# Performance work log

Measured on AMD Instinct MI355X. Metric: run time of the kernel, lower is better.

## Reference

```python
import jax, jax.numpy as jnp
import numpy as np

N = 100_000   # total nodes in batched graph
E = 800_000   # total edges
D = 64        # in_dim
H = 64        # hidden_dim
C = 10        # out_dim (num classes)
L = 3         # num_layers
G = 500       # graphs in batch
EPS = 1e-5    # BatchNorm eps


def setup_inputs() -> dict:
    key = jax.random.key(0)
    ks = jax.random.split(key, 12)
    feat = jax.random.normal(ks[0], (N, D), dtype=jnp.float32)
    src = jax.random.randint(ks[1], (E,), 0, N, dtype=jnp.int32)
    dst = jax.random.randint(ks[2], (E,), 0, N, dtype=jnp.int32)
    node2graph = jnp.sort(jax.random.randint(ks[3], (N,), 0, G, dtype=jnp.int32))
    # stacked GCN layer params (in_dim == hidden_dim so all layers share shape)
    Ws = jax.random.normal(ks[4], (L, H, H), dtype=jnp.float32) * 0.1
    bs = jax.random.normal(ks[5], (L, H), dtype=jnp.float32) * 0.01
    gammas = 1.0 + 0.1 * jax.random.normal(ks[6], (L, H), dtype=jnp.float32)
    betas = 0.1 * jax.random.normal(ks[7], (L, H), dtype=jnp.float32)
    means = 0.1 * jax.random.normal(ks[8], (L, H), dtype=jnp.float32)
    vars_ = jax.random.uniform(ks[9], (L, H), dtype=jnp.float32) + 0.5
    Wc = jax.random.normal(ks[10], (H, C), dtype=jnp.float32) * 0.1
    bc = jax.random.normal(ks[11], (C,), dtype=jnp.float32) * 0.01
    return {"feat": feat, "src": src, "dst": dst, "node2graph": node2graph,
            "Ws": Ws, "bs": bs, "gammas": gammas, "betas": betas,
            "means": means, "vars_": vars_, "Wc": Wc, "bc": bc}


def reference(feat, src, dst, node2graph, Ws, bs, gammas, betas, means, vars_, Wc, bc):
    h = feat
    for l in range(L):
        # dgl copy_src + sum: aggregate source features at destination nodes
        m = jax.ops.segment_sum(h[src], dst, num_segments=N)  # [N, H]
        h = m @ Ws[l] + bs[l]                                  # Linear
        # BatchNorm1d (eval mode, running stats)
        h = (h - means[l]) * (gammas[l] / jnp.sqrt(vars_[l] + EPS)) + betas[l]
        h = jax.nn.elu(h)
    logits = h @ Wc + bc                    # classify(h)
    logp = jax.nn.log_softmax(logits, axis=1)
    Hent = -jnp.sum(jnp.exp(logp) * logp, axis=1)   # entropy per node
    lam = 1.0 - Hent / jnp.max(Hent)                # lambda_list
    # ragged per-graph weighted sum pooling
    pooled = jax.ops.segment_sum(lam[:, None] * h, node2graph, num_segments=G)  # [G, H]
    return pooled @ Wc + bc                 # final classify (dropout eval = id)
```

## Files before the change

kernel.cpp:

```cpp
#include <hip/hip_runtime.h>
#include <hip/hip_bf16.h>
#include <math.h>

#define NNODES 100000
#define NEDGES 800000
#define HDIM 64
#define CDIM 10
#define NGRAPH 500
#define CAP 24
#define OVFCAP 16384
#define BN_EPS 1e-5f
#define TN 64

typedef __attribute__((ext_vector_type(8))) short short8;
typedef __attribute__((ext_vector_type(4))) float f32x4;

__device__ __forceinline__ float bflo(unsigned u){ return __uint_as_float(u << 16); }
__device__ __forceinline__ float bfhi(unsigned u){ return __uint_as_float(u & 0xFFFF0000u); }
__device__ __forceinline__ unsigned f2bf(float f){
    unsigned u = __float_as_uint(f);
    u += 0x7FFFu + ((u >> 16) & 1u);
    return u >> 16;
}

__global__ void cvt_feat(const float4* __restrict__ F, uint4* __restrict__ B) {
    int i = blockIdx.x * 256 + threadIdx.x;
    float4 a = F[2*i], b = F[2*i+1];
    uint4 o;
    o.x = f2bf(a.x) | (f2bf(a.y) << 16);
    o.y = f2bf(a.z) | (f2bf(a.w) << 16);
    o.z = f2bf(b.x) | (f2bf(b.y) << 16);
    o.w = f2bf(b.z) | (f2bf(b.w) << 16);
    B[i] = o;
}

__global__ void fill_buckets(const int* __restrict__ src, const int* __restrict__ dst,
                             unsigned* __restrict__ cnt, int* __restrict__ csr,
                             unsigned* __restrict__ ovfcnt, int* __restrict__ ovf) {
    int e = blockIdx.x * blockDim.x + threadIdx.x;
    if (e >= NEDGES) return;
    int d = dst[e];
    unsigned slot = atomicAdd(&cnt[d], 1u);
    if (slot < CAP) {
        csr[(size_t)d * CAP + slot] = src[e];
    } else {
        unsigned o = atomicAdd(ovfcnt, 1u);
        if (o < OVFCAP) { ovf[2*o] = src[e]; ovf[2*o+1] = d; }
    }
}

__global__ __launch_bounds__(256, 6) void layer_fused(
        const unsigned* __restrict__ hb, const unsigned* __restrict__ cnt,
        const int* __restrict__ csr, const unsigned* __restrict__ ovfcnt,
        const int* __restrict__ ovf,
        const float* __restrict__ Ws, const float* __restrict__ bs,
        const float* __restrict__ gammas, const float* __restrict__ betas,
        const float* __restrict__ means, const float* __restrict__ vars_,
        int layer, unsigned short* __restrict__ out16) {
    __shared__ unsigned short Mb[TN][72];
    __shared__ unsigned short Wt[HDIM][72];
    __shared__ float Scl[HDIM], Shl[HDIM];
    int tid = threadIdx.x;
    int base = blockIdx.x * TN;

    const float* Wg = Ws + (size_t)layer*HDIM*HDIM;
    #pragma unroll
    for (int r = 0; r < 16; ++r) {
        int f = tid + 256*r;
        int k = f >> 6, c = f & 63;
        Wt[c][k] = (unsigned short)f2bf(Wg[f]);
    }
    if (tid < HDIM) {
        int c = tid;
        float b  = bs[layer*HDIM + c];
        float gm = gammas[layer*HDIM + c];
        float be = betas[layer*HDIM + c];
        float mu = means[layer*HDIM + c];
        float vv = vars_[layer*HDIM + c];
        float s  = gm * rsqrtf(vv + BN_EPS);
        Scl[c] = s;
        Shl[c] = (b - mu) * s + be;
    }

    int grp = tid >> 3;
    int sub = tid & 7;
    const uint4* h4 = (const uint4*)hb;
    unsigned novf = *ovfcnt; if (novf > OVFCAP) novf = OVFCAP;
    #pragma unroll
    for (int i = 0; i < 2; ++i) {
        int row = grp + 32*i;
        int node = base + row;
        float a0=0,a1=0,a2=0,a3=0,a4=0,a5=0,a6=0,a7=0;
        if (node < NNODES) {
            unsigned deg = cnt[node]; if (deg > CAP) deg = CAP;
            const int* ed = csr + (size_t)node * CAP;
            unsigned e = 0;
            for (; e + 4 <= deg; e += 4) {
                int s0 = ed[e], s1 = ed[e+1], s2 = ed[e+2], s3 = ed[e+3];
                uint4 v0 = h4[(size_t)s0*8 + sub];
                uint4 v1 = h4[(size_t)s1*8 + sub];
                uint4 v2 = h4[(size_t)s2*8 + sub];
                uint4 v3 = h4[(size_t)s3*8 + sub];
                a0 += bflo(v0.x)+bflo(v1.x)+bflo(v2.x)+bflo(v3.x);
                a1 += bfhi(v0.x)+bfhi(v1.x)+bfhi(v2.x)+bfhi(v3.x);
                a2 += bflo(v0.y)+bflo(v1.y)+bflo(v2.y)+bflo(v3.y);
                a3 += bfhi(v0.y)+bfhi(v1.y)+bfhi(v2.y)+bfhi(v3.y);
                a4 += bflo(v0.z)+bflo(v1.z)+bflo(v2.z)+bflo(v3.z);
                a5 += bfhi(v0.z)+bfhi(v1.z)+bfhi(v2.z)+bfhi(v3.z);
                a6 += bflo(v0.w)+bflo(v1.w)+bflo(v2.w)+bflo(v3.w);
                a7 += bfhi(v0.w)+bfhi(v1.w)+bfhi(v2.w)+bfhi(v3.w);
            }
            for (; e < deg; ++e) {
                uint4 v = h4[(size_t)ed[e]*8 + sub];
                a0 += bflo(v.x); a1 += bfhi(v.x);
                a2 += bflo(v.y); a3 += bfhi(v.y);
                a4 += bflo(v.z); a5 += bfhi(v.z);
                a6 += bflo(v.w); a7 += bfhi(v.w);
            }
            if (novf) {
                for (unsigned o = 0; o < novf; ++o) {
                    if (ovf[2*o+1] == node) {
                        uint4 v = h4[(size_t)ovf[2*o]*8 + sub];
                        a0 += bflo(v.x); a1 += bfhi(v.x);
                        a2 += bflo(v.y); a3 += bfhi(v.y);
                        a4 += bflo(v.z); a5 += bfhi(v.z);
                        a6 += bflo(v.w); a7 += bfhi(v.w);
                    }
                }
            }
        }
        uint4 p;
        p.x = f2bf(a0) | (f2bf(a1) << 16);
        p.y = f2bf(a2) | (f2bf(a3) << 16);
        p.z = f2bf(a4) | (f2bf(a5) << 16);
        p.w = f2bf(a6) | (f2bf(a7) << 16);
        *(uint4*)&Mb[row][sub*8] = p;
    }
    __syncthreads();

    int w  = tid >> 6;
    int l  = tid & 63;
    int lr = l & 15;
    int lq = l >> 4;
    short8 a0 = *(const short8*)&Mb[w*16 + lr][lq*8];
    short8 a1 = *(const short8*)&Mb[w*16 + lr][32 + lq*8];
    f32x4 acc0 = {0.f,0.f,0.f,0.f}, acc1 = acc0, acc2 = acc0, acc3 = acc0;
    {
        short8 b0 = *(const short8*)&Wt[ 0 + lr][lq*8];
        short8 b1 = *(const short8*)&Wt[ 0 + lr][32 + lq*8];
        acc0 = __builtin_amdgcn_mfma_f32_16x16x32_bf16(a0, b0, acc0, 0, 0, 0);
        acc0 = __builtin_amdgcn_mfma_f32_16x16x32_bf16(a1, b1, acc0, 0, 0, 0);
    }
    {
        short8 b0 = *(const short8*)&Wt[16 + lr][lq*8];
        short8 b1 = *(const short8*)&Wt[16 + lr][32 + lq*8];
        acc1 = __builtin_amdgcn_mfma_f32_16x16x32_bf16(a0, b0, acc1, 0, 0, 0);
        acc1 = __builtin_amdgcn_mfma_f32_16x16x32_bf16(a1, b1, acc1, 0, 0, 0);
    }
    {
        short8 b0 = *(const short8*)&Wt[32 + lr][lq*8];
        short8 b1 = *(const short8*)&Wt[32 + lr][32 + lq*8];
        acc2 = __builtin_amdgcn_mfma_f32_16x16x32_bf16(a0, b0, acc2, 0, 0, 0);
        acc2 = __builtin_amdgcn_mfma_f32_16x16x32_bf16(a1, b1, acc2, 0, 0, 0);
    }
    {
        short8 b0 = *(const short8*)&Wt[48 + lr][lq*8];
        short8 b1 = *(const short8*)&Wt[48 + lr][32 + lq*8];
        acc3 = __builtin_amdgcn_mfma_f32_16x16x32_bf16(a0, b0, acc3, 0, 0, 0);
        acc3 = __builtin_amdgcn_mfma_f32_16x16x32_bf16(a1, b1, acc3, 0, 0, 0);
    }

    #pragma unroll
    for (int t = 0; t < 4; ++t) {
        f32x4 a = (t==0)?acc0:(t==1)?acc1:(t==2)?acc2:acc3;
        int col = t*16 + lr;
        float s = Scl[col], sh = Shl[col];
        #pragma unroll
        for (int r = 0; r < 4; ++r) {
            int node = base + w*16 + lq*4 + r;
            if (node < NNODES) {
                float y = a[r]*s + sh;
                y = (y > 0.f) ? y : expm1f(y);
                out16[(size_t)node*HDIM + col] = (unsigned short)f2bf(y);
            }
        }
    }
}

__global__ __launch_bounds__(256) void classify_bf16(
        const uint4* __restrict__ h4, const float* __restrict__ Wc,
        const float* __restrict__ bc, float* __restrict__ Hent,
        unsigned* __restrict__ maxH) {
    __shared__ float Wl[HDIM*11];
    __shared__ float bl[CDIM];
    __shared__ float wmax[4];
    int tid = threadIdx.x;
    for (int idx = tid; idx < HDIM*CDIM; idx += 256)
        Wl[(idx/CDIM)*11 + (idx%CDIM)] = Wc[idx];
    if (tid < CDIM) bl[tid] = bc[tid];
    __syncthreads();

    int node = blockIdx.x * 32 + (tid >> 3);
    int sub  = tid & 7;
    uint4 v = h4[(size_t)node*8 + sub];
    float h[8];
    h[0]=bflo(v.x); h[1]=bfhi(v.x); h[2]=bflo(v.y); h[3]=bfhi(v.y);
    h[4]=bflo(v.z); h[5]=bfhi(v.z); h[6]=bflo(v.w); h[7]=bfhi(v.w);

    float lg[CDIM];
    #pragma unroll
    for (int c = 0; c < CDIM; ++c) lg[c] = 0.f;
    #pragma unroll
    for (int k = 0; k < 8; ++k) {
        const float* wr = &Wl[(sub*8 + k)*11];
        float x = h[k];
        #pragma unroll
        for (int c = 0; c < CDIM; ++c) lg[c] += x * wr[c];
    }
    #pragma unroll
    for (int m = 1; m < 8; m <<= 1)
        #pragma unroll
        for (int c = 0; c < CDIM; ++c) lg[c] += __shfl_xor(lg[c], m, 64);
    #pragma unroll
    for (int c = 0; c < CDIM; ++c) lg[c] += bl[c];

    float mx = lg[0];
    #pragma unroll
    for (int c = 1; c < CDIM; ++c) mx = fmaxf(mx, lg[c]);
    float se = 0.f, dot = 0.f;
    #pragma unroll
    for (int c = 0; c < CDIM; ++c) { float e = expf(lg[c]-mx); se += e; dot += e*lg[c]; }
    float Hv = (mx + logf(se)) - dot/se;
    Hv = fmaxf(Hv, 0.f);
    if (sub == 0) Hent[node] = Hv;

    float m8 = Hv;
    #pragma unroll
    for (int m = 8; m < 64; m <<= 1) m8 = fmaxf(m8, __shfl_xor(m8, m, 64));
    if ((tid & 63) == 0) wmax[tid >> 6] = m8;
    __syncthreads();
    if (tid == 0) {
        float mm = fmaxf(fmaxf(wmax[0], wmax[1]), fmaxf(wmax[2], wmax[3]));
        atomicMax(maxH, __float_as_uint(mm));
    }
}

__global__ void pool_final_bf16(const unsigned* __restrict__ H2, const float* __restrict__ Hent,
                                const unsigned* __restrict__ maxH, const int* __restrict__ n2g,
                                const float* __restrict__ Wc, const float* __restrict__ bc,
                                float* __restrict__ out) {
    __shared__ float partial[8][HDIM];
    __shared__ float pooled[HDIM];
    int g = blockIdx.x;
    int tid = threadIdx.x;

    int lo = 0, hi = NNODES;
    while (lo < hi) { int mid = (lo+hi) >> 1; if (n2g[mid] < g) lo = mid+1; else hi = mid; }
    int start = lo;
    hi = NNODES;
    while (lo < hi) { int mid = (lo+hi) >> 1; if (n2g[mid] < g+1) lo = mid+1; else hi = mid; }
    int end = lo;

    float invMax = 1.0f / __uint_as_float(*maxH);
    int half = tid >> 5, l = tid & 31;
    float ax = 0.f, ay = 0.f;
    for (int i = start + half; i < end; i += 8) {
        float lam = 1.0f - Hent[i] * invMax;
        unsigned u = H2[(size_t)i*32 + l];
        ax += lam * bflo(u);
        ay += lam * bfhi(u);
    }
    partial[half][2*l]   = ax;
    partial[half][2*l+1] = ay;
    __syncthreads();
    if (tid < HDIM) {
        float s = 0.f;
        #pragma unroll
        for (int hh = 0; hh < 8; ++hh) s += partial[hh][tid];
        pooled[tid] = s;
    }
    __syncthreads();
    if (tid < CDIM) {
        float s = bc[tid];
        for (int k = 0; k < HDIM; ++k) s += pooled[k] * Wc[k*CDIM + tid];
        out[g*CDIM + tid] = s;
    }
}

extern "C" void kernel_launch(void* const* d_in, const int* in_sizes, int n_in,
                              void* d_out, int out_size, void* d_ws, size_t ws_size,
                              hipStream_t stream) {
    const float* feat  = (const float*)d_in[0];
    const int*   src   = (const int*)d_in[1];
    const int*   dst   = (const int*)d_in[2];
    const int*   n2g   = (const int*)d_in[3];
    const float* Ws    = (const float*)d_in[4];
    const float* bs    = (const float*)d_in[5];
    const float* gam   = (const float*)d_in[6];
    const float* bet   = (const float*)d_in[7];
    const float* mea   = (const float*)d_in[8];
    const float* var_  = (const float*)d_in[9];
    const float* Wc    = (const float*)d_in[10];
    const float* bc    = (const float*)d_in[11];
    float* out = (float*)d_out;

    char* ws = (char*)d_ws;
    size_t off = 0;
    auto take = [&](size_t bytes) {
        char* p = ws + off;
        off += (bytes + 255) & ~(size_t)255;
        return p;
    };

    unsigned* cnt    = (unsigned*)take((size_t)NNODES*4);
    unsigned* ovfcnt = (unsigned*)take(4);
    unsigned* maxH   = (unsigned*)take(4);
    int*      ovf    = (int*)take((size_t)OVFCAP*2*4);
    float*    Hent   = (float*)take((size_t)NNODES*4);
    unsigned* featb  = (unsigned*)take((size_t)NNODES*HDIM*2);
    unsigned* HA     = (unsigned*)take((size_t)NNODES*HDIM*2);
    unsigned* HB     = (unsigned*)take((size_t)NNODES*HDIM*2);
    int*      csr    = (int*)take((size_t)NNODES*CAP*4);

    hipMemsetAsync(cnt, 0, (size_t)NNODES*4, stream);
    hipMemsetAsync(ovfcnt, 0, 4, stream);
    hipMemsetAsync(maxH, 0, 4, stream);

    cvt_feat<<<(NNODES*HDIM/8 + 255)/256, 256, 0, stream>>>((const float4*)feat, (uint4*)featb);
    fill_buckets<<<(NEDGES+255)/256, 256, 0, stream>>>(src, dst, cnt, csr, ovfcnt, ovf);

    int grid = (NNODES + TN - 1) / TN;
    layer_fused<<<grid, 256, 0, stream>>>(featb, cnt, csr, ovfcnt, ovf,
                                          Ws, bs, gam, bet, mea, var_, 0, (unsigned short*)HA);
    layer_fused<<<grid, 256, 0, stream>>>((const unsigned*)HA, cnt, csr, ovfcnt, ovf,
                                          Ws, bs, gam, bet, mea, var_, 1, (unsigned short*)HB);
    layer_fused<<<grid, 256, 0, stream>>>((const unsigned*)HB, cnt, csr, ovfcnt, ovf,
                                          Ws, bs, gam, bet, mea, var_, 2, (unsigned short*)HA);

    classify_bf16<<<(NNODES+31)/32, 256, 0, stream>>>((const uint4*)HA, Wc, bc, Hent, maxH);
    pool_final_bf16<<<NGRAPH, 256, 0, stream>>>(HA, Hent, maxH, n2g, Wc, bc, out);
}
```

Measured before the change: 196.2 us.

## Build CSR via two-pass binning with shared-memory bucket assembly

Replaces the per-node global-atomic bucket fill with a two-pass scheme. First, edges are scattered into 128-node bins using padded per-bin counters, fused with the feature bf16 conversion. Then one block per bin assembles the node buckets in shared memory and writes the CSR out with coalesced stores. This is meant to cut scattered global atomics and writes, and it removes the large memset of per-node counters. It also raises layer_fused launch bounds to 8 waves per SIMD, which risks register spills and relies on bins not exceeding BINCAP (overflow falls back to the ovf list).

Result: no change. 194.0 us (-1.1%).

```diff
diff --git a/kernel.cpp b/kernel.cpp
--- a/kernel.cpp
+++ b/kernel.cpp
@@ -11,6 +11,9 @@
 #define OVFCAP 16384
 #define BN_EPS 1e-5f
 #define TN 64
+#define NBINS 782
+#define BINCAP 2048
+#define GCUR_STRIDE 16
 
 typedef __attribute__((ext_vector_type(8))) short short8;
 typedef __attribute__((ext_vector_type(4))) float f32x4;
@@ -23,7 +26,10 @@
     return u >> 16;
 }
 
-__global__ void cvt_feat(const float4* __restrict__ F, uint4* __restrict__ B) {
+__global__ void prep(const float4* __restrict__ F, uint4* __restrict__ B,
+                     const int* __restrict__ src, const int* __restrict__ dst,
+                     unsigned* __restrict__ gcur, unsigned* __restrict__ bin_edges,
+                     unsigned* __restrict__ ovfcnt, int* __restrict__ ovf) {
     int i = blockIdx.x * 256 + threadIdx.x;
     float4 a = F[2*i], b = F[2*i+1];
     uint4 o;
@@ -32,24 +38,45 @@
     o.z = f2bf(b.x) | (f2bf(b.y) << 16);
     o.w = f2bf(b.z) | (f2bf(b.w) << 16);
     B[i] = o;
-}
-
-__global__ void fill_buckets(const int* __restrict__ src, const int* __restrict__ dst,
-                             unsigned* __restrict__ cnt, int* __restrict__ csr,
-                             unsigned* __restrict__ ovfcnt, int* __restrict__ ovf) {
-    int e = blockIdx.x * blockDim.x + threadIdx.x;
-    if (e >= NEDGES) return;
-    int d = dst[e];
-    unsigned slot = atomicAdd(&cnt[d], 1u);
-    if (slot < CAP) {
-        csr[(size_t)d * CAP + slot] = src[e];
-    } else {
-        unsigned o = atomicAdd(ovfcnt, 1u);
-        if (o < OVFCAP) { ovf[2*o] = src[e]; ovf[2*o+1] = d; }
-    }
-}
-
-__global__ __launch_bounds__(256, 6) void layer_fused(
+    int d = dst[i], s = src[i];
+    int bin = d >> 7;
+    unsigned pos = atomicAdd(&gcur[bin * GCUR_STRIDE], 1u);
+    unsigned u = ((unsigned)(d & 127) << 24) | (unsigned)s;
+    if (pos < BINCAP) bin_edges[(size_t)bin * BINCAP + pos] = u;
+    else { unsigned oo = atomicAdd(ovfcnt, 1u);
+           if (oo < OVFCAP) { ovf[2*oo] = s; ovf[2*oo+1] = d; } }
+}
+
+__global__ __launch_bounds__(256) void build_csr(
+        const unsigned* __restrict__ gcur, const unsigned* __restrict__ bin_edges,
+        unsigned* __restrict__ cnt, int* __restrict__ csr,
+        unsigned* __restrict__ ovfcnt, int* __restrict__ ovf) {
+    __shared__ unsigned lcnt[128];
+    __shared__ __align__(16) int lcsr[128][CAP];
+    int p = blockIdx.x, tid = threadIdx.x;
+    if (tid < 128) lcnt[tid] = 0;
+    __syncthreads();
+    unsigned ecnt = gcur[p * GCUR_STRIDE]; if (ecnt > BINCAP) ecnt = BINCAP;
+    for (unsigned i = tid; i < ecnt; i += 256) {
+        unsigned u = bin_edges[(size_t)p * BINCAP + i];
+        unsigned ln = u >> 24; int s = (int)(u & 0xFFFFFFu);
+        unsigned slot = atomicAdd(&lcnt[ln], 1u);
+        if (slot < CAP) lcsr[ln][slot] = s;
+        else {
+            unsigned oo = atomicAdd(ovfcnt, 1u);
+            if (oo < OVFCAP) { ovf[2*oo] = s; ovf[2*oo+1] = (p << 7) + (int)ln; }
+        }
+    }
+    __syncthreads();
+    int node = (p << 7) + tid;
+    if (tid < 128 && node < NNODES) cnt[node] = lcnt[tid];
+    const uint4* ls = (const uint4*)&lcsr[0][0];
+    uint4* gs = (uint4*)(csr + (size_t)(p << 7) * CAP);
+    #pragma unroll
+    for (int i = tid; i < 128*CAP/4; i += 256) gs[i] = ls[i];
+}
+
+__global__ __launch_bounds__(256, 8) void layer_fused(
         const unsigned* __restrict__ hb, const unsigned* __restrict__ cnt,
         const int* __restrict__ csr, const unsigned* __restrict__ ovfcnt,
         const int* __restrict__ ovf,
@@ -129,12 +156,12 @@
                 }
             }
         }
-        uint4 p;
-        p.x = f2bf(a0) | (f2bf(a1) << 16);
-        p.y = f2bf(a2) | (f2bf(a3) << 16);
-        p.z = f2bf(a4) | (f2bf(a5) << 16);
-        p.w = f2bf(a6) | (f2bf(a7) << 16);
-        *(uint4*)&Mb[row][sub*8] = p;
+        uint4 pk;
+        pk.x = f2bf(a0) | (f2bf(a1) << 16);
+        pk.y = f2bf(a2) | (f2bf(a3) << 16);
+        pk.z = f2bf(a4) | (f2bf(a5) << 16);
+        pk.w = f2bf(a6) | (f2bf(a7) << 16);
+        *(uint4*)&Mb[row][sub*8] = pk;
     }
     __syncthreads();
 
@@ -312,22 +339,25 @@
         return p;
     };
 
-    unsigned* cnt    = (unsigned*)take((size_t)NNODES*4);
-    unsigned* ovfcnt = (unsigned*)take(4);
-    unsigned* maxH   = (unsigned*)take(4);
-    int*      ovf    = (int*)take((size_t)OVFCAP*2*4);
-    float*    Hent   = (float*)take((size_t)NNODES*4);
-    unsigned* featb  = (unsigned*)take((size_t)NNODES*HDIM*2);
-    unsigned* HA     = (unsigned*)take((size_t)NNODES*HDIM*2);
-    unsigned* HB     = (unsigned*)take((size_t)NNODES*HDIM*2);
-    int*      csr    = (int*)take((size_t)NNODES*CAP*4);
-
-    hipMemsetAsync(cnt, 0, (size_t)NNODES*4, stream);
+    unsigned* gcur     = (unsigned*)take((size_t)NBINS*GCUR_STRIDE*4);
+    unsigned* ovfcnt   = (unsigned*)take(4);
+    unsigned* maxH     = (unsigned*)take(4);
+    int*      ovf      = (int*)take((size_t)OVFCAP*2*4);
+    float*    Hent     = (float*)take((size_t)NNODES*4);
+    unsigned* featb    = (unsigned*)take((size_t)NNODES*HDIM*2);
+    unsigned* HA       = (unsigned*)take((size_t)NNODES*HDIM*2);
+    unsigned* HB       = (unsigned*)take((size_t)NNODES*HDIM*2);
+    unsigned* bin_edges= (unsigned*)take((size_t)NBINS*BINCAP*4);
+    unsigned* cnt      = (unsigned*)take((size_t)NNODES*4);
+    int*      csr      = (int*)take((size_t)NBINS*128*CAP*4);
+
+    hipMemsetAsync(gcur, 0, (size_t)NBINS*GCUR_STRIDE*4, stream);
     hipMemsetAsync(ovfcnt, 0, 4, stream);
     hipMemsetAsync(maxH, 0, 4, stream);
 
-    cvt_feat<<<(NNODES*HDIM/8 + 255)/256, 256, 0, stream>>>((const float4*)feat, (uint4*)featb);
-    fill_buckets<<<(NEDGES+255)/256, 256, 0, stream>>>(src, dst, cnt, csr, ovfcnt, ovf);
+    prep<<<NEDGES/256, 256, 0, stream>>>((const float4*)feat, (uint4*)featb,
+                                         src, dst, gcur, bin_edges, ovfcnt, ovf);
+    build_csr<<<NBINS, 256, 0, stream>>>(gcur, bin_edges, cnt, csr, ovfcnt, ovf);
 
     int grid = (NNODES + TN - 1) / TN;
     layer_fused<<<grid, 256, 0, stream>>>(featb, cnt, csr, ovfcnt, ovf,
```
